# Kernel tuning notes

Hardware: AMD Instinct MI355X
Metric: run time of the kernel (lower is better)

## Reference

```python
import jax, jax.numpy as jnp
import numpy as np
from jax import lax

# 32 binary morphology kernels, row-major bit strings (kernel01..kernel800)
K3S = ["111001111", "111101101", "111100111", "101101111",
       "011101111", "111101011", "111101110", "110101111"]
K4S = ["0011000110011111", "1100100010011111", "1111100100010011", "1111100110001100",
       "1001100110011111", "1111000100011111", "1111100110011001", "1111100010001111"]
K5S = ["0001100001000011000111111", "1100010000100001000111111",
       "1111110001100001000011000", "1111110001000010000100011",
       "1111110000100001000011111", "1111100001000010000111111",
       "1111110001100011000110001", "1000110001100011000111111"]
K6S = ["000011000001000001000001100001111111", "110000100000100000100000100001111111",
       "111111100001100000100000100000110000", "111111100001000001000001000001000011",
       "111111100000100000100000100000111111", "111111000001000001000001000001111111",
       "111111100001100001100001100001100001", "100001100001100001100001100001111111"]

def _mk(strs, k):
    a = np.array([[int(c) for c in s] for s in strs], dtype=np.float32)
    return jnp.asarray(a.reshape(len(strs), 1, k, k))

# 'thick' mode: enumerate(start=1) vs set(range(32)) drops the LAST kernel (index 31)
GROUPS = [_mk(K3S, 3), _mk(K4S, 4), _mk(K5S, 5), _mk(K6S, 6)[:7]]

DIA = jnp.ones((1, 1, 3, 3), jnp.float32)
ERO = jnp.asarray([[0, 1, 0], [1, 0, 1], [0, 1, 0]], jnp.float32).reshape(1, 1, 3, 3)

def _conv(x, k, pad):
    return lax.conv_general_dilated(x, k, (1, 1), ((pad, pad), (pad, pad)),
                                    dimension_numbers=("NCHW", "OIHW", "NCHW"))

def _sig2(x, beta=0.5, alpha=10.0):
    # 1 / (1 + exp(-alpha*(x - beta)))
    return jax.nn.sigmoid(alpha * (x - beta))

def _endpoints_group(padded, kers):
    # batch all same-size kernels as output channels of one conv
    k = kers.shape[-1]
    pad = k // 2
    nc = _conv(padded, kers, pad)
    nc = nc[:, :, :padded.shape[2], :padded.shape[3]]  # crop (even-size kernels overshoot)
    # soft_threshold(nc, 1.0) * mask
    le = jax.nn.sigmoid(jnp.clip(-10.0 * (nc - 1.0), -10.0, 10.0)) * padded
    return le[:, :, 1:-1, 1:-1].sum(axis=1, keepdims=True)

def _cp_map(t):
    p = jnp.pad(t, ((0, 0), (0, 0), (1, 1), (1, 1)), constant_values=1.0)
    epss = _endpoints_group(p, GROUPS[0])
    for K in GROUPS[1:]:
        epss = epss + _endpoints_group(p, K)
    return _sig2(epss)

def _dilate(x):
    return jnp.clip(_conv(x, DIA, 1), 0.0, 1.0)

def _erode(x):
    t = _conv(x, ERO, 1)
    return _sig2(t / (t.max() + 1e-8), beta=0.7, alpha=10.0)

def _get_cp(t):
    return _dilate(_cp_map(t))

def _topo_loss(pred, gt, num_erosions):
    ge, pe = [gt], [pred]
    for _ in range(num_erosions):
        ge.append(_erode(ge[-1]))
        pe.append(_erode(pe[-1]))
    loss = jnp.float32(0.0)
    for i in range(num_erosions + 1):
        loss = loss + ((_get_cp(pe[i]) - _get_cp(ge[i])) ** 2).sum()
        loss = loss + ((_get_cp(pe[i].max() - pe[i]) - _get_cp(ge[i].max() - ge[i])) ** 2).sum()
    return loss / pred.shape[0]


def setup_inputs() -> dict:
    key = jax.random.key(0)
    k1, k2 = jax.random.split(key)
    B, H, W = 8, 512, 512
    pred = jax.random.uniform(k1, (B, 1, H, W), dtype=jnp.float32)
    gt = jax.random.uniform(k2, (B, 1, H, W), dtype=jnp.float32)
    return {"pred": pred, "gt": gt, "num_erosions": 2}


def reference(pred, gt, num_erosions):
    return _topo_loss(pred, gt, num_erosions)
```

## Files before the change

kernel.cpp:

```cpp
#include <hip/hip_runtime.h>
#include <hip/hip_fp16.h>
#include <cstdint>

static constexpr int B = 8;
static constexpr int H = 512;
static constexpr int W = 512;
static constexpr int HW = H * W;
static constexpr int NPIX = B * HW;
static constexpr int NB1 = 1024;
static constexpr int NBD = 1024;

static constexpr int N_INT = 30 * 14;
static constexpr int N_EDGE = 64 + 120;
static constexpr int GRID_X = N_INT + N_EDGE;

static constexpr float CC = 14.4269504088896f;

__device__ __forceinline__ float rcpf(float x) { return __builtin_amdgcn_rcpf(x); }
__device__ __forceinline__ float exp2f_n(float x) { return __builtin_amdgcn_exp2f(x); }

typedef __attribute__((ext_vector_type(2))) float f2;

__device__ __forceinline__ f2 mk2(float a, float b) { f2 r; r.x = a; r.y = b; return r; }
__device__ __forceinline__ f2 exp2_2(f2 v) {
    f2 r; r.x = exp2f_n(v.x); r.y = exp2f_n(v.y); return r;
}
__device__ __forceinline__ f2 rcp_2(f2 v) {
    f2 r; r.x = rcpf(v.x); r.y = rcpf(v.y); return r;
}
#if defined(__has_builtin)
#if __has_builtin(__builtin_elementwise_fma)
#define FMA2(a, b, c) __builtin_elementwise_fma((a), (b), (c))
#endif
#endif
#ifndef FMA2
__device__ __forceinline__ f2 fma2_(f2 a, f2 b, f2 c) {
    f2 r; r.x = fmaf(a.x, b.x, c.x); r.y = fmaf(a.y, b.y, c.y); return r;
}
#define FMA2(a, b, c) fma2_((a), (b), (c))
#endif

__device__ __forceinline__ float sig_cp(float x) {
    return rcpf(1.0f + exp2f_n(fmaf(x, -CC, 0.5f * CC)));
}
__device__ __forceinline__ float sig_er(float r) {
    return rcpf(1.0f + exp2f_n(fmaf(r, -CC, 0.7f * CC)));
}
__device__ __forceinline__ void pair_term2(f2 nc, f2 negA, f2 s2m,
                                           f2& sd, f2& sc) {
    const f2 CC2 = CC;
    const f2 one2 = 1.0f;
    f2 w = exp2_2(FMA2(nc, CC2, negA));
    sd += rcp_2(FMA2(w, s2m, one2));
    sc += w * rcp_2(w + s2m);
}
__device__ __forceinline__ void end_term2(f2 nc, f2& sd) {
    const f2 CC2 = CC;
    const f2 nCC2 = -CC;
    const f2 one2 = 1.0f;
    sd += rcp_2(one2 + exp2_2(FMA2(nc, CC2, nCC2)));
}
__device__ __forceinline__ float wave_max(float m) {
#pragma unroll
    for (int o = 32; o > 0; o >>= 1) m = fmaxf(m, __shfl_down(m, o, 64));
    return m;
}
__device__ __forceinline__ float wave_sum(float s) {
#pragma unroll
    for (int o = 32; o > 0; o >>= 1) s += __shfl_down(s, o, 64);
    return s;
}

union H4 {
    uint64_t u;
    __half2 h2[2];
    __half h[4];
};

__device__ __forceinline__ float4 h4_to_f4(uint64_t u) {
    H4 v; v.u = u;
    float2 p0 = __half22float2(v.h2[0]);
    float2 p1 = __half22float2(v.h2[1]);
    return make_float4(p0.x, p0.y, p1.x, p1.y);
}
__device__ __forceinline__ float4 f4_add(float4 a, float4 b) {
    return make_float4(a.x + b.x, a.y + b.y, a.z + b.z, a.w + b.w);
}

struct NC2 {
    f2 n3[8], n4[8], n5[8], n6[7];
    f2 v;
};

template <int STRIDE>
__device__ __forceinline__ NC2 sweep2(const f2* rp) {
    NC2 o;
    f2 r2s, r3s, r4s;
    f2 cen0, cen1, cen2, cen3, cen4, cen5, cen6, cen7, cen8;
    {
        f2 c0 = rp[0], c1 = rp[1], c2 = rp[2], c3 = rp[3], c4 = rp[4], c5 = rp[5];
        f2 c45 = c4 + c5, c01 = c0 + c1;
        f2 S6 = (c01 + (c2 + c3)) + c45;
        o.n6[0] = c45; o.n6[1] = c01; o.n6[2] = S6; o.n6[3] = S6;
        o.n6[4] = S6;  o.n6[5] = S6;  o.n6[6] = S6;
    }
    rp += STRIDE;
    {
        f2 c0 = rp[0], c1 = rp[1], c2 = rp[2], c3 = rp[3], c4 = rp[4], c5 = rp[5];
        f2 c45 = c4 + c5, c12 = c1 + c2, c34 = c3 + c4;
        f2 S4 = c12 + c34, S5 = S4 + c5;
        f2 c15 = c1 + c5, c05 = c0 + c5, c14 = c1 + c4;
        o.n6[0] += c5;  o.n6[1] += c0;  o.n6[2] += c05; o.n6[3] += c05;
        o.n6[4] += c0;  o.n6[5] += c5;  o.n6[6] += c05;
        o.n5[0] = c45; o.n5[1] = c12; o.n5[2] = S5; o.n5[3] = S5;
        o.n5[4] = S5;  o.n5[5] = S5;  o.n5[6] = S5; o.n5[7] = c15;
        o.n4[0] = c34; o.n4[1] = c12; o.n4[2] = S4; o.n4[3] = S4;
        o.n4[4] = c14; o.n4[5] = S4;  o.n4[6] = S4; o.n4[7] = S4;
    }
    rp += STRIDE;
    {
        f2 c0 = rp[0], c1 = rp[1], c2 = rp[2], c3 = rp[3], c4 = rp[4], c5 = rp[5];
        f2 c05 = c0 + c5, c15 = c1 + c5, c14 = c1 + c4;
        r2s = (c2 + c3) + c4;
        cen0 = c2; cen1 = c3; cen2 = c4;
        o.n6[0] += c5;  o.n6[1] += c0;  o.n6[2] += c0;  o.n6[3] += c5;
        o.n6[4] += c0;  o.n6[5] += c5;  o.n6[6] += c05;
        o.n5[0] += c5;  o.n5[1] += c1;  o.n5[2] += c15; o.n5[3] += c15;
        o.n5[4] += c1;  o.n5[5] += c5;  o.n5[6] += c15; o.n5[7] += c15;
        o.n4[0] += c4;  o.n4[1] += c1;  o.n4[2] += c14; o.n4[3] += c14;
        o.n4[4] += c14; o.n4[5] += c4;  o.n4[6] += c14; o.n4[7] += c1;
    }
    rp += STRIDE;
    {
        f2 c0 = rp[0], c1 = rp[1], c2 = rp[2], c3 = rp[3], c4 = rp[4], c5 = rp[5];
        f2 c05 = c0 + c5, c15 = c1 + c5, c14 = c1 + c4;
        r3s = (c2 + c3) + c4;
        cen3 = c2; cen4 = c3; cen5 = c4;
        o.v = c3;
        o.n6[0] += c5;  o.n6[1] += c0;  o.n6[2] += c0;  o.n6[3] += c5;
        o.n6[4] += c0;  o.n6[5] += c5;  o.n6[6] += c05;
        o.n5[0] += c5;  o.n5[1] += c1;  o.n5[2] += c1;  o.n5[3] += c5;
        o.n5[4] += c1;  o.n5[5] += c5;  o.n5[6] += c15; o.n5[7] += c15;
        o.n4[0] += c14; o.n4[1] += c14; o.n4[2] += c4;  o.n4[3] += c1;
        o.n4[4] += c14; o.n4[5] += c4;  o.n4[6] += c14; o.n4[7] += c1;
    }
    rp += STRIDE;
    {
        f2 c0 = rp[0], c1 = rp[1], c2 = rp[2], c3 = rp[3], c4 = rp[4], c5 = rp[5];
        f2 c05 = c0 + c5, c15 = c1 + c5, c12 = c1 + c2, c34 = c3 + c4;
        f2 S4 = c12 + c34, c14 = c1 + c4;
        r4s = (c2 + c3) + c4;
        cen6 = c2; cen7 = c3; cen8 = c4;
        o.n6[0] += c05; o.n6[1] += c05; o.n6[2] += c0;  o.n6[3] += c5;
        o.n6[4] += c0;  o.n6[5] += c5;  o.n6[6] += c05;
        o.n5[0] += c15; o.n5[1] += c15; o.n5[2] += c1;  o.n5[3] += c5;
        o.n5[4] += c1;  o.n5[5] += c5;  o.n5[6] += c15; o.n5[7] += c15;
        o.n4[0] += S4;  o.n4[1] += S4;  o.n4[2] += c34; o.n4[3] += c12;
        o.n4[4] += S4;  o.n4[5] += S4;  o.n4[6] += c14; o.n4[7] += S4;
    }
    rp += STRIDE;
    {
        f2 c0 = rp[0], c1 = rp[1], c2 = rp[2], c3 = rp[3], c4 = rp[4], c5 = rp[5];
        f2 c45 = c4 + c5, c12 = c1 + c2;
        f2 t = c3 + c45, S5 = c12 + t, S6 = S5 + c0;
        f2 c01 = c0 + c1, c05 = c0 + c5, c15 = c1 + c5;
        o.n6[0] += S6;  o.n6[1] += S6;  o.n6[2] += c01; o.n6[3] += c45;
        o.n6[4] += S6;  o.n6[5] += S6;  o.n6[6] += c05;
        o.n5[0] += S5;  o.n5[1] += S5;  o.n5[2] += c12; o.n5[3] += c45;
        o.n5[4] += S5;  o.n5[5] += S5;  o.n5[6] += c15; o.n5[7] += S5;
    }
    f2 S33 = (r2s + r3s) + r4s;
    f2 T = S33 - cen4;
    o.n3[0] = T - cen3; o.n3[1] = T - cen7; o.n3[2] = T - cen5; o.n3[3] = T - cen1;
    o.n3[4] = T - cen0; o.n3[5] = T - cen6; o.n3[6] = T - cen8; o.n3[7] = T - cen2;
    return o;
}

__constant__ __device__ const int CI4[8] = {1, 1, 1, 1, 2, 2, 2, 2};
__constant__ __device__ const int CI5[8] = {3, 3, 3, 3, 4, 4, 4, 4};
__constant__ __device__ const int CI6[7] = {4, 4, 4, 4, 5, 5, 5};

template <bool PAIR>
__device__ __forceinline__ void ssum_from_nc2(const NC2& a, const f2* negA,
                                              const f2* s2m, f2& sD, f2& sC) {
    f2 sd = 0.0f, sc = 0.0f;
#pragma unroll
    for (int k = 0; k < 8; k++) {
        if constexpr (PAIR) pair_term2(a.n3[k], negA[0], s2m[0], sd, sc);
        else end_term2(a.n3[k], sd);
    }
#pragma unroll
    for (int k = 0; k < 8; k++) {
        if constexpr (PAIR) pair_term2(a.n4[k], negA[CI4[k]], s2m[CI4[k]], sd, sc);
        else end_term2(a.n4[k], sd);
    }
#pragma unroll
    for (int k = 0; k < 8; k++) {
        if constexpr (PAIR) pair_term2(a.n5[k], negA[CI5[k]], s2m[CI5[k]], sd, sc);
        else end_term2(a.n5[k], sd);
    }
#pragma unroll
    for (int k = 0; k < 7; k++) {
        if constexpr (PAIR) pair_term2(a.n6[k], negA[CI6[k]], s2m[CI6[k]], sd, sc);
        else end_term2(a.n6[k], sd);
    }
    sD = sd;
    sC = sc;
}

__global__ __launch_bounds__(256, 4) void cp_main_kernel(
    const float* __restrict__ x0P, const float* __restrict__ x0G,
    const float* __restrict__ x1P, const float* __restrict__ x1G,
    const float* __restrict__ x2P, const float* __restrict__ x2G,
    const float* __restrict__ S, const float* __restrict__ CST,
    int lvl_base, int plane_lvl0, __half* __restrict__ cp) {
    __shared__ f2 win[37][23];
    const int lvl = lvl_base + (blockIdx.z >> 3);
    const int b = blockIdx.z & 7;
    const float* xP = (lvl == 0) ? x0P : (lvl == 1) ? x1P : x2P;
    const float* xG = (lvl == 0) ? x0G : (lvl == 1) ? x1G : x2G;
    const float MP = S[lvl], MG = S[3 + lvl];
    __half* cpb = cp + (size_t)(4 * (lvl - plane_lvl0)) * NPIX;
    const int tid = threadIdx.y * 16 + threadIdx.x;
    const int ty = threadIdx.y, tx = threadIdx.x;
    const f2* cbase = (const f2*)(CST + lvl * 24);

    if (blockIdx.x < N_INT) {
        const int txB = 1 + (int)blockIdx.x % 30;
        const int tyB = 1 + (int)blockIdx.x / 30;
        const int ox0 = txB * 16, oy0 = tyB * 32;
        const float* pb = xP + b * HW + (oy0 - 3) * W + (ox0 - 3);
        const float* gb = xG + b * HW + (oy0 - 3) * W + (ox0 - 3);
        {
            int i = tid, r = tid / 21, c = tid - (tid / 21) * 21;
            while (i < 37 * 21) {
                win[r][c] = mk2(pb[r * W + c], gb[r * W + c]);
                i += 256; c += 4; r += 12;
                if (c >= 21) { c -= 21; r += 1; }
            }
        }
        __syncthreads();
        f2 negA[6], s2m[6];
#pragma unroll
        for (int c = 0; c < 6; c++) { negA[c] = cbase[c]; s2m[c] = cbase[6 + c]; }
        int o = b * HW + (oy0 + ty) * W + (ox0 + tx);
        {
            f2 sd, sc;
            NC2 a = sweep2<23>(&win[ty][tx]);
            ssum_from_nc2<true>(a, negA, s2m, sd, sc);
            H4 v;
            v.h[0] = __float2half(sig_cp(a.v.x * sd.x));
            v.h[1] = __float2half(sig_cp(a.v.y * sd.y));
            v.h[2] = __float2half(sig_cp((MP - a.v.x) * sc.x));
            v.h[3] = __float2half(sig_cp((MG - a.v.y) * sc.y));
            *(uint64_t*)(cpb + (size_t)o * 4) = v.u;
        }
        o += 16 * W;
        {
            f2 sd, sc;
            NC2 a = sweep2<23>(&win[ty + 16][tx]);
            ssum_from_nc2<true>(a, negA, s2m, sd, sc);
            H4 v;
            v.h[0] = __float2half(sig_cp(a.v.x * sd.x));
            v.h[1] = __float2half(sig_cp(a.v.y * sd.y));
            v.h[2] = __float2half(sig_cp((MP - a.v.x) * sc.x));
            v.h[3] = __float2half(sig_cp((MG - a.v.y) * sc.y));
            *(uint64_t*)(cpb + (size_t)o * 4) = v.u;
        }
    } else {
        const int e = (int)blockIdx.x - N_INT;
        int tx16, ty16;
        if (e < 64) {
            ty16 = e >> 1;
            tx16 = (e & 1) ? 31 : 0;
        } else {
            int e2 = e - 64;
            int r = e2 / 30;
            ty16 = (r == 0) ? 0 : (r == 1) ? 1 : (r == 2) ? 30 : 31;
            tx16 = 1 + e2 % 30;
        }
        const int ox0 = tx16 * 16, oy0 = ty16 * 16;
        const int o = b * HW + (oy0 + ty) * W + (ox0 + tx);
        const bool fastw = (tx16 >= 1) & (tx16 <= 30) & (ty16 >= 1) & (ty16 <= 30);
        if (fastw) {
            const float* pb = xP + b * HW + (oy0 - 3) * W + (ox0 - 3);
            const float* gb = xG + b * HW + (oy0 - 3) * W + (ox0 - 3);
            {
                int i = tid, r = tid / 21, c = tid - (tid / 21) * 21;
                while (i < 21 * 21) {
                    win[r][c] = mk2(pb[r * W + c], gb[r * W + c]);
                    i += 256; c += 4; r += 12;
                    if (c >= 21) { c -= 21; r += 1; }
                }
            }
            __syncthreads();
            f2 negA[6], s2m[6], sd, sc;
#pragma unroll
            for (int c = 0; c < 6; c++) { negA[c] = cbase[c]; s2m[c] = cbase[6 + c]; }
            NC2 a = sweep2<23>(&win[ty][tx]);
            ssum_from_nc2<true>(a, negA, s2m, sd, sc);
            H4 v;
            v.h[0] = __float2half(sig_cp(a.v.x * sd.x));
            v.h[1] = __float2half(sig_cp(a.v.y * sd.y));
            v.h[2] = __float2half(sig_cp((MP - a.v.x) * sc.x));
            v.h[3] = __float2half(sig_cp((MG - a.v.y) * sc.y));
            *(uint64_t*)(cpb + (size_t)o * 4) = v.u;
        } else {
            const float* pb = xP + b * HW;
            const float* gb = xG + b * HW;
            {
                int i = tid, r = tid / 21, c = tid - (tid / 21) * 21;
                while (i < 21 * 21) {
                    int pr = oy0 - 2 + r;
                    int pc = ox0 - 2 + c;
                    f2 v;
                    if (pr < 0 || pr > H + 1 || pc < 0 || pc > W + 1) {
                        v = 0.0f;
                    } else if (pr == 0 || pr == H + 1 || pc == 0 || pc == W + 1) {
                        v = 1.0f;
                    } else {
                        v = mk2(pb[(pr - 1) * W + (pc - 1)], gb[(pr - 1) * W + (pc - 1)]);
                    }
                    win[r][c] = v;
                    i += 256; c += 4; r += 12;
                    if (c >= 21) { c -= 21; r += 1; }
                }
            }
            __syncthreads();
            f2 sd, sc, junk;
            NC2 a = sweep2<23>(&win[ty][tx]);
            ssum_from_nc2<false>(a, nullptr, nullptr, sd, junk);
            f2 vD = a.v;
            __half2* po = (__half2*)(cpb + (size_t)o * 4);
            po[0] = __halves2half2(__float2half(sig_cp(vD.x * sd.x)),
                                   __float2half(sig_cp(vD.y * sd.y)));
            __syncthreads();
            {
                int i = tid, r = tid / 21, c = tid - (tid / 21) * 21;
                while (i < 21 * 21) {
                    int pr = oy0 - 2 + r;
                    int pc = ox0 - 2 + c;
                    f2 v;
                    if (pr < 0 || pr > H + 1 || pc < 0 || pc > W + 1) {
                        v = 0.0f;
                    } else if (pr == 0 || pr == H + 1 || pc == 0 || pc == W + 1) {
                        v = 1.0f;
                    } else {
                        v = mk2(MP - pb[(pr - 1) * W + (pc - 1)],
                                MG - gb[(pr - 1) * W + (pc - 1)]);
                    }
                    win[r][c] = v;
                    i += 256; c += 4; r += 12;
                    if (c >= 21) { c -= 21; r += 1; }
                }
            }
            __syncthreads();
            NC2 ac = sweep2<23>(&win[ty][tx]);
            ssum_from_nc2<false>(ac, nullptr, nullptr, sc, junk);
            po[1] = __halves2half2(__float2half(sig_cp(ac.v.x * sc.x)),
                                   __float2half(sig_cp(ac.v.y * sc.y)));
        }
    }
}

__global__ __launch_bounds__(256, 4) void dil_diff2_kernel(
    const __half* __restrict__ cp, float* __restrict__ partial) {
    const int plane_grp = blockIdx.x >> 9;
    const int r = blockIdx.x & 511;
    const __half* cpb = cp + (size_t)(4 * plane_grp) * NPIX;
    const int x0 = threadIdx.x << 1;
    const int y0 = (r & 63) << 3;
    const int b = r >> 6;
    const __half* pb = cpb + (size_t)b * HW * 4;

    float4 ring0[3], ring1[3];
    float s = 0.0f;
#pragma unroll
    for (int j = 0; j < 10; j++) {
        int yy = y0 - 1 + j;
        float4 a0 = make_float4(0.f, 0.f, 0.f, 0.f);
        float4 a1 = a0;
        if (yy >= 0 && yy < H) {
            const __half* row = pb + (size_t)yy * (W * 4);
            float4 f0 = h4_to_f4(*(const uint64_t*)(row + (size_t)x0 * 4));
            float4 f1 = h4_to_f4(*(const uint64_t*)(row + (size_t)(x0 + 1) * 4));
            float4 lf = make_float4(0.f, 0.f, 0.f, 0.f), rt = lf;
            if (x0 > 0)
                lf = h4_to_f4(*(const uint64_t*)(row + (size_t)(x0 - 1) * 4));
            if (x0 + 2 < W)
                rt = h4_to_f4(*(const uint64_t*)(row + (size_t)(x0 + 2) * 4));
            a0 = f4_add(f4_add(lf, f0), f1);
            a1 = f4_add(f4_add(f0, f1), rt);
        }
        ring0[j % 3] = a0; ring1[j % 3] = a1;
        if (j >= 2) {
            float4 v0 = f4_add(f4_add(ring0[(j - 2) % 3], ring0[(j - 1) % 3]),
                               ring0[j % 3]);
            float4 v1 = f4_add(f4_add(ring1[(j - 2) % 3], ring1[(j - 1) % 3]),
                               ring1[j % 3]);
            float d1 = fminf(v0.x, 1.0f) - fminf(v0.y, 1.0f);
            float d2 = fminf(v0.z, 1.0f) - fminf(v0.w, 1.0f);
            s += fmaf(d1, d1, d2 * d2);
            d1 = fminf(v1.x, 1.0f) - fminf(v1.y, 1.0f);
            d2 = fminf(v1.z, 1.0f) - fminf(v1.w, 1.0f);
            s += fmaf(d1, d1, d2 * d2);
        }
    }
    s = wave_sum(s);
    __shared__ float red[4];
    int tid = threadIdx.x;
    if ((tid & 63) == 0) red[tid >> 6] = s;
    __syncthreads();
    if (tid == 0) partial[blockIdx.x] = (red[0] + red[1]) + (red[2] + red[3]);
}

__device__ __forceinline__ void cross4(const float* __restrict__ xp, int idx,
                                       int y, int c, float4& ctr, float t[4]) {
    const float4* v = (const float4*)(xp + idx);
    ctr = v[0];
    float4 up = (y > 0) ? *(const float4*)(xp + idx - W)
                        : make_float4(0, 0, 0, 0);
    float4 dn = (y < H - 1) ? *(const float4*)(xp + idx + W)
                            : make_float4(0, 0, 0, 0);
    float lf = (c > 0) ? xp[idx - 1] : 0.0f;
    float rt = (c < W - 4) ? xp[idx + 4] : 0.0f;
    t[0] = (up.x + dn.x) + (lf + ctr.y);
    t[1] = (up.y + dn.y) + (ctr.x + ctr.z);
    t[2] = (up.z + dn.z) + (ctr.y + ctr.w);
    t[3] = (up.w + dn.w) + (ctr.z + rt);
}

__device__ __forceinline__ void cross_lds(const float* rm1, const float* r0,
                                          const float* rp1, int col,
                                          float4& ctr, float t[4]) {
    ctr = *(const float4*)(r0 + col);
    float4 up = *(const float4*)(rm1 + col);
    float4 dn = *(const float4*)(rp1 + col);
    float lf = (col > 0) ? r0[col - 1] : 0.0f;
    float rt = (col < W - 4) ? r0[col + 4] : 0.0f;
    t[0] = (up.x + dn.x) + (lf + ctr.y);
    t[1] = (up.y + dn.y) + (ctr.x + ctr.z);
    t[2] = (up.z + dn.z) + (ctr.y + ctr.w);
    t[3] = (up.w + dn.w) + (ctr.z + rt);
}

__global__ __launch_bounds__(256) void cross_max_both_kernel(
    const float* __restrict__ xP, const float* __restrict__ xG,
    float4* __restrict__ partial) {
    float mtP = 0, mtG = 0, mrP = 0, mrG = 0;
    for (int T = blockIdx.x * 256 + threadIdx.x; T < NPIX / 4; T += NB1 * 256) {
        int idx = T * 4;
        int i = idx & (HW - 1);
        int y = i >> 9;
        int c = i & (W - 1);
        float4 ctr;
        float t[4];
        cross4(xP, idx, y, c, ctr, t);
        mtP = fmaxf(mtP, fmaxf(fmaxf(t[0], t[1]), fmaxf(t[2], t[3])));
        mrP = fmaxf(mrP, fmaxf(fmaxf(ctr.x, ctr.y), fmaxf(ctr.z, ctr.w)));
        cross4(xG, idx, y, c, ctr, t);
        mtG = fmaxf(mtG, fmaxf(fmaxf(t[0], t[1]), fmaxf(t[2], t[3])));
        mrG = fmaxf(mrG, fmaxf(fmaxf(ctr.x, ctr.y), fmaxf(ctr.z, ctr.w)));
    }
    mtP = wave_max(mtP); mtG = wave_max(mtG);
    mrP = wave_max(mrP); mrG = wave_max(mrG);
    __shared__ float red[4][4];
    int tid = threadIdx.x;
    if ((tid & 63) == 0) {
        int w = tid >> 6;
        red[w][0] = mtP; red[w][1] = mtG; red[w][2] = mrP; red[w][3] = mrG;
    }
    __syncthreads();
    if (tid == 0) {
        float4 r;
        r.x = fmaxf(fmaxf(red[0][0], red[1][0]), fmaxf(red[2][0], red[3][0]));
        r.y = fmaxf(fmaxf(red[0][1], red[1][1]), fmaxf(red[2][1], red[3][1]));
        r.z = fmaxf(fmaxf(red[0][2], red[1][2]), fmaxf(red[2][2], red[3][2]));
        r.w = fmaxf(fmaxf(red[0][3], red[1][3]), fmaxf(red[2][3], red[3][3]));
        partial[blockIdx.x] = r;
    }
}

__global__ __launch_bounds__(256) void erode_cmax_kernel(
    const float* __restrict__ xP, const float* __restrict__ xG,
    const float4* __restrict__ PM1,
    float* __restrict__ yP, float* __restrict__ yG,
    float4* __restrict__ PMo, float* __restrict__ S) {
    __shared__ float lyP[6][W], lyG[6][W];
    __shared__ float red[4][4];
    const int tid = threadIdx.x;
    const int b = blockIdx.x >> 7;
    const int y0 = ((int)blockIdx.x & 127) << 2;

    float a = 0, bm = 0, c4 = 0, d4 = 0;
#pragma unroll
    for (int k = 0; k < NB1 / 256; k++) {
        float4 p = PM1[tid + k * 256];
        a = fmaxf(a, p.x); bm = fmaxf(bm, p.y);
        c4 = fmaxf(c4, p.z); d4 = fmaxf(d4, p.w);
    }
    a = wave_max(a); bm = wave_max(bm); c4 = wave_max(c4); d4 = wave_max(d4);
    if ((tid & 63) == 0) {
        int w = tid >> 6;
        red[w][0] = a; red[w][1] = bm; red[w][2] = c4; red[w][3] = d4;
    }
    __syncthreads();
    a  = fmaxf(fmaxf(red[0][0], red[1][0]), fmaxf(red[2][0], red[3][0]));
    bm = fmaxf(fmaxf(red[0][1], red[1][1]), fmaxf(red[2][1], red[3][1]));
    c4 = fmaxf(fmaxf(red[0][2], red[1][2]), fmaxf(red[2][2], red[3][2]));
    d4 = fmaxf(fmaxf(red[0][3], red[1][3]), fmaxf(red[2][3], red[3][3]));
    const float invP = rcpf(a + 1e-8f);
    const float invG = rcpf(bm + 1e-8f);

    for (int t = tid; t < 6 * 128; t += 256) {
        int ri = t >> 7;
        int col = (t & 127) << 2;
        int yy = y0 - 1 + ri;
        float4 oP = make_float4(0.f, 0.f, 0.f, 0.f), oG = oP;
        if (yy >= 0 && yy < H) {
            int idx = b * HW + yy * W + col;
            float4 ctr; float tv[4];
            cross4(xP, idx, yy, col, ctr, tv);
            oP = make_float4(sig_er(tv[0] * invP), sig_er(tv[1] * invP),
                             sig_er(tv[2] * invP), sig_er(tv[3] * invP));
            cross4(xG, idx, yy, col, ctr, tv);
            oG = make_float4(sig_er(tv[0] * invG), sig_er(tv[1] * invG),
                             sig_er(tv[2] * invG), sig_er(tv[3] * invG));
            if (ri >= 1 && ri <= 4) {
                *(float4*)(yP + idx) = oP;
                *(float4*)(yG + idx) = oG;
            }
        }
        *(float4*)(&lyP[ri][col]) = oP;
        *(float4*)(&lyG[ri][col]) = oG;
    }
    __syncthreads();

    float mtP = 0, mtG = 0, mrP = 0, mrG = 0;
    for (int t = tid; t < 4 * 128; t += 256) {
        int rj = 1 + (t >> 7);
        int col = (t & 127) << 2;
        float4 ctr; float tv[4];
        cross_lds(lyP[rj - 1], lyP[rj], lyP[rj + 1], col, ctr, tv);
        mtP = fmaxf(mtP, fmaxf(fmaxf(tv[0], tv[1]), fmaxf(tv[2], tv[3])));
        mrP = fmaxf(mrP, fmaxf(fmaxf(ctr.x, ctr.y), fmaxf(ctr.z, ctr.w)));
        cross_lds(lyG[rj - 1], lyG[rj], lyG[rj + 1], col, ctr, tv);
        mtG = fmaxf(mtG, fmaxf(fmaxf(tv[0], tv[1]), fmaxf(tv[2], tv[3])));
        mrG = fmaxf(mrG, fmaxf(fmaxf(ctr.x, ctr.y), fmaxf(ctr.z, ctr.w)));
    }
    mtP = wave_max(mtP); mtG = wave_max(mtG);
    mrP = wave_max(mrP); mrG = wave_max(mrG);
    __syncthreads();
    if ((tid & 63) == 0) {
        int w = tid >> 6;
        red[w][0] = mtP; red[w][1] = mtG; red[w][2] = mrP; red[w][3] = mrG;
    }
    __syncthreads();
    if (tid == 0) {
        float4 r;
        r.x = fmaxf(fmaxf(red[0][0], red[1][0]), fmaxf(red[2][0], red[3][0]));
        r.y = fmaxf(fmaxf(red[0][1], red[1][1]), fmaxf(red[2][1], red[3][1]));
        r.z = fmaxf(fmaxf(red[0][2], red[1][2]), fmaxf(red[2][2], red[3][2]));
        r.w = fmaxf(fmaxf(red[0][3], red[1][3]), fmaxf(red[2][3], red[3][3]));
        PMo[blockIdx.x] = r;
        if (blockIdx.x == 0) {
            S[1] = sig_er(a * invP);
            S[4] = sig_er(bm * invG);
            S[0] = c4;
            S[3] = d4;
        }
    }
}

__global__ __launch_bounds__(256) void erode_both_kernel(
    const float* __restrict__ xP, const float* __restrict__ xG,
    const float4* __restrict__ PM,
    float* __restrict__ yP, float* __restrict__ yG,
    float* ymaxP, float* ymaxG, float* rmaxP, float* rmaxG,
    const float* __restrict__ Sg, float* __restrict__ CST) {
    float a = 0, bm = 0, c4 = 0, d4 = 0;
    {
        int t = threadIdx.x;
#pragma unroll
        for (int k = 0; k < NB1 / 256; k++) {
            float4 p = PM[t + k * 256];
            a = fmaxf(a, p.x); bm = fmaxf(bm, p.y);
            c4 = fmaxf(c4, p.z); d4 = fmaxf(d4, p.w);
        }
        a = wave_max(a); bm = wave_max(bm); c4 = wave_max(c4); d4 = wave_max(d4);
        __shared__ float red[4][4];
        if ((t & 63) == 0) {
            int w = t >> 6;
            red[w][0] = a; red[w][1] = bm; red[w][2] = c4; red[w][3] = d4;
        }
        __syncthreads();
        a  = fmaxf(fmaxf(red[0][0], red[1][0]), fmaxf(red[2][0], red[3][0]));
        bm = fmaxf(fmaxf(red[0][1], red[1][1]), fmaxf(red[2][1], red[3][1]));
        c4 = fmaxf(fmaxf(red[0][2], red[1][2]), fmaxf(red[2][2], red[3][2]));
        d4 = fmaxf(fmaxf(red[0][3], red[1][3]), fmaxf(red[2][3], red[3][3]));
    }
    const float tP_max = a, tG_max = bm;
    const float invP = rcpf(tP_max + 1e-8f);
    const float invG = rcpf(tG_max + 1e-8f);

    const int T = blockIdx.x * 256 + threadIdx.x;
    if (T < NPIX / 4) {
        int idx = T * 4;
        int i = idx & (HW - 1);
        int y = i >> 9;
        int c = i & (W - 1);
        float4 ctr;
        float t[4], o[4];
        cross4(xP, idx, y, c, ctr, t);
#pragma unroll
        for (int k = 0; k < 4; k++) o[k] = sig_er(t[k] * invP);
        *(float4*)(yP + idx) = make_float4(o[0], o[1], o[2], o[3]);
        cross4(xG, idx, y, c, ctr, t);
#pragma unroll
        for (int k = 0; k < 4; k++) o[k] = sig_er(t[k] * invG);
        *(float4*)(yG + idx) = make_float4(o[0], o[1], o[2], o[3]);
    }
    if (blockIdx.x == 0) {
        if (threadIdx.x == 0) {
            *ymaxP = sig_er(tP_max * invP);
            *ymaxG = sig_er(tG_max * invG);
            *rmaxP = c4;
            *rmaxG = d4;
        }
        if (threadIdx.x < 36) {
            int t = threadIdx.x;
            int lvl = t / 12, rem = t % 12, cls = rem >> 1, img = rem & 1;
            const float cntf[6] = {7.0f, 9.0f, 10.0f, 11.0f, 13.0f, 16.0f};
            float M;
            if (lvl == 2)
                M = img ? sig_er(tG_max * invG) : sig_er(tP_max * invP);
            else
                M = Sg[lvl + 3 * img];
            float cm = fmaf(cntf[cls] * M, CC, -CC);
            float m = 0.5f * (cm - CC);
            CST[lvl * 24 + cls * 2 + img] = -(CC + m);
            CST[lvl * 24 + 12 + cls * 2 + img] = exp2f_n(m);
        }
    }
}

__global__ __launch_bounds__(1024) void finalize_kernel(
    const float* __restrict__ PS, float* out) {
    int t = threadIdx.x;
    float s = PS[t] + ((t < 512) ? PS[t + 1024] : 0.0f);
    s = wave_sum(s);
    __shared__ float red[16];
    if ((t & 63) == 0) red[t >> 6] = s;
    __syncthreads();
    if (t == 0) {
        float tot = 0.0f;
#pragma unroll
        for (int i = 0; i < 16; i++) tot += red[i];
        out[0] = tot * (1.0f / (float)B);
    }
}

extern "C" void kernel_launch(void* const* d_in, const int* in_sizes, int n_in,
                              void* d_out, int out_size, void* d_ws, size_t ws_size,
                              hipStream_t stream) {
    (void)in_sizes; (void)n_in; (void)out_size;
    const float* pred = (const float*)d_in[0];
    const float* gt   = (const float*)d_in[1];
    float* out = (float*)d_out;

    float* S  = (float*)d_ws;
    float4* PM = (float4*)(S + 64);
    float* PS = S + 64 + 4 * NB1;
    float* CST = PS + 2560;
    float* P1 = PS + 3 * NBD;
    float* G1 = P1 + NPIX;
    float* P2 = G1 + NPIX;
    float* G2 = P2 + NPIX;
    __half* CP = (__half*)(G2 + NPIX);
    float4* PM2 = (float4*)CP;

    const size_t base_b = (size_t)(64 + 4 * NB1 + 3 * NBD) * 4 +
                          (size_t)4 * NPIX * 4;
    const bool merged = ws_size >= base_b + (size_t)12 * NPIX * 2;

    const dim3 b1(256), g1(NB1), gE(NPIX / 4 / 256);
    const dim3 b2(16, 16, 1);

    cross_max_both_kernel<<<g1, b1, 0, stream>>>(pred, gt, PM);
    erode_cmax_kernel<<<dim3(NB1), b1, 0, stream>>>(pred, gt, PM, P1, G1,
                                                    PM2, S);
    erode_both_kernel<<<gE, b1, 0, stream>>>(P1, G1, PM2, P2, G2,
                                             S + 2, S + 5, S + 12, S + 13,
                                             S, CST);

    if (merged) {
        cp_main_kernel<<<dim3(GRID_X, 1, 3 * B), b2, 0, stream>>>(
            pred, gt, P1, G1, P2, G2, S, CST, 0, 0, CP);
        dil_diff2_kernel<<<dim3(3 * 512), b1, 0, stream>>>(CP, PS);
    } else {
        for (int lvl = 0; lvl < 3; lvl++) {
            cp_main_kernel<<<dim3(GRID_X, 1, B), b2, 0, stream>>>(
                pred, gt, P1, G1, P2, G2, S, CST, lvl, lvl, CP);
            dil_diff2_kernel<<<dim3(512), b1, 0, stream>>>(CP, PS + lvl * 512);
        }
    }

    finalize_kernel<<<1, 1024, 0, stream>>>(PS, out);
}
```

Baseline: 251.6 us.

## Fuse second erosion into cp_main tile loads, dropping erode_both kernel

Removes the separate kernel that materialised the second-level eroded images P2/G2. For level 2, cp_main now reduces the per-block maxima itself and computes the erosion on the fly while filling its shared-memory window. The per-level pair constants are also derived in-block. This saves a full-image write and read pass plus one launch, at the cost of redundant erosion arithmetic and extra halo gathers in every level-2 block, plus a small per-block max reduction.

```diff
diff --git a/kernel.cpp b/kernel.cpp
--- a/kernel.cpp
+++ b/kernel.cpp
@@ -85,6 +85,20 @@
 }
 __device__ __forceinline__ float4 f4_add(float4 a, float4 b) {
     return make_float4(a.x + b.x, a.y + b.y, a.z + b.z, a.w + b.w);
+}
+
+__device__ __forceinline__ float erode_at(const float* __restrict__ p,
+                                          int y, int x, float inv) {
+    int i = y * W + x;
+    float up = (y > 0) ? p[i - W] : 0.0f;
+    float dn = (y < H - 1) ? p[i + W] : 0.0f;
+    float lf = (x > 0) ? p[i - 1] : 0.0f;
+    float rt = (x < W - 1) ? p[i + 1] : 0.0f;
+    return sig_er(((up + dn) + (lf + rt)) * inv);
+}
+__device__ __forceinline__ float erode_at_i(const float* __restrict__ p,
+                                            int i, float inv) {
+    return sig_er(((p[i - W] + p[i + W]) + (p[i - 1] + p[i + 1])) * inv);
 }
 
 struct NC2 {
@@ -208,22 +222,64 @@
     sC = sc;
 }
 
+__device__ __forceinline__ void pair_const(float cnt, float M,
+                                           float& negA, float& s2m) {
+    float cm = fmaf(cnt * M, CC, -CC);
+    float m = 0.5f * (cm - CC);
+    negA = -(CC + m);
+    s2m = exp2f_n(m);
+}
+
 __global__ __launch_bounds__(256, 4) void cp_main_kernel(
     const float* __restrict__ x0P, const float* __restrict__ x0G,
     const float* __restrict__ x1P, const float* __restrict__ x1G,
-    const float* __restrict__ x2P, const float* __restrict__ x2G,
+    const float4* __restrict__ PM2,
     const float* __restrict__ S, const float* __restrict__ CST,
     int lvl_base, int plane_lvl0, __half* __restrict__ cp) {
     __shared__ f2 win[37][23];
+    __shared__ float redc[4][2];
     const int lvl = lvl_base + (blockIdx.z >> 3);
     const int b = blockIdx.z & 7;
-    const float* xP = (lvl == 0) ? x0P : (lvl == 1) ? x1P : x2P;
-    const float* xG = (lvl == 0) ? x0G : (lvl == 1) ? x1G : x2G;
-    const float MP = S[lvl], MG = S[3 + lvl];
+    const bool l2 = (lvl == 2);
+    const float* xP = (lvl == 0) ? x0P : x1P;
+    const float* xG = (lvl == 0) ? x0G : x1G;
     __half* cpb = cp + (size_t)(4 * (lvl - plane_lvl0)) * NPIX;
     const int tid = threadIdx.y * 16 + threadIdx.x;
     const int ty = threadIdx.y, tx = threadIdx.x;
-    const f2* cbase = (const f2*)(CST + lvl * 24);
+
+    float MP, MG, invP2 = 0.0f, invG2 = 0.0f;
+    f2 negA[6], s2m[6];
+    if (!l2) {
+        MP = S[lvl]; MG = S[3 + lvl];
+        const f2* cbase = (const f2*)(CST + lvl * 24);
+#pragma unroll
+        for (int c = 0; c < 6; c++) { negA[c] = cbase[c]; s2m[c] = cbase[6 + c]; }
+    } else {
+        float a = 0.0f, bm = 0.0f;
+#pragma unroll
+        for (int k = 0; k < NB1 / 256; k++) {
+            float4 p = PM2[tid + k * 256];
+            a = fmaxf(a, p.x); bm = fmaxf(bm, p.y);
+        }
+        a = wave_max(a); bm = wave_max(bm);
+        if ((tid & 63) == 0) { redc[tid >> 6][0] = a; redc[tid >> 6][1] = bm; }
+        __syncthreads();
+        a  = fmaxf(fmaxf(redc[0][0], redc[1][0]), fmaxf(redc[2][0], redc[3][0]));
+        bm = fmaxf(fmaxf(redc[0][1], redc[1][1]), fmaxf(redc[2][1], redc[3][1]));
+        invP2 = rcpf(a + 1e-8f);
+        invG2 = rcpf(bm + 1e-8f);
+        MP = sig_er(a * invP2);
+        MG = sig_er(bm * invG2);
+        const float cntf[6] = {7.0f, 9.0f, 10.0f, 11.0f, 13.0f, 16.0f};
+#pragma unroll
+        for (int c = 0; c < 6; c++) {
+            float nP, sP, nG, sG;
+            pair_const(cntf[c], MP, nP, sP);
+            pair_const(cntf[c], MG, nG, sG);
+            negA[c] = mk2(nP, nG);
+            s2m[c] = mk2(sP, sG);
+        }
+    }
 
     if (blockIdx.x < N_INT) {
         const int txB = 1 + (int)blockIdx.x % 30;
@@ -231,18 +287,24 @@
         const int ox0 = txB * 16, oy0 = tyB * 32;
         const float* pb = xP + b * HW + (oy0 - 3) * W + (ox0 - 3);
         const float* gb = xG + b * HW + (oy0 - 3) * W + (ox0 - 3);
-        {
+        if (!l2) {
             int i = tid, r = tid / 21, c = tid - (tid / 21) * 21;
             while (i < 37 * 21) {
                 win[r][c] = mk2(pb[r * W + c], gb[r * W + c]);
                 i += 256; c += 4; r += 12;
                 if (c >= 21) { c -= 21; r += 1; }
             }
+        } else {
+            int i = tid, r = tid / 21, c = tid - (tid / 21) * 21;
+            while (i < 37 * 21) {
+                int idx = r * W + c;
+                win[r][c] = mk2(erode_at_i(pb, idx, invP2),
+                                erode_at_i(gb, idx, invG2));
+                i += 256; c += 4; r += 12;
+                if (c >= 21) { c -= 21; r += 1; }
+            }
         }
         __syncthreads();
-        f2 negA[6], s2m[6];
-#pragma unroll
-        for (int c = 0; c < 6; c++) { negA[c] = cbase[c]; s2m[c] = cbase[6 + c]; }
         int o = b * HW + (oy0 + ty) * W + (ox0 + tx);
         {
             f2 sd, sc;
@@ -285,18 +347,25 @@
         if (fastw) {
             const float* pb = xP + b * HW + (oy0 - 3) * W + (ox0 - 3);
             const float* gb = xG + b * HW + (oy0 - 3) * W + (ox0 - 3);
-            {
+            if (!l2) {
                 int i = tid, r = tid / 21, c = tid - (tid / 21) * 21;
                 while (i < 21 * 21) {
                     win[r][c] = mk2(pb[r * W + c], gb[r * W + c]);
                     i += 256; c += 4; r += 12;
                     if (c >= 21) { c -= 21; r += 1; }
                 }
+            } else {
+                int i = tid, r = tid / 21, c = tid - (tid / 21) * 21;
+                while (i < 21 * 21) {
+                    int idx = r * W + c;
+                    win[r][c] = mk2(erode_at_i(pb, idx, invP2),
+                                    erode_at_i(gb, idx, invG2));
+                    i += 256; c += 4; r += 12;
+                    if (c >= 21) { c -= 21; r += 1; }
+                }
             }
             __syncthreads();
-            f2 negA[6], s2m[6], sd, sc;
-#pragma unroll
-            for (int c = 0; c < 6; c++) { negA[c] = cbase[c]; s2m[c] = cbase[6 + c]; }
+            f2 sd, sc;
             NC2 a = sweep2<23>(&win[ty][tx]);
             ssum_from_nc2<true>(a, negA, s2m, sd, sc);
             H4 v;
@@ -318,8 +387,11 @@
                         v = 0.0f;
                     } else if (pr == 0 || pr == H + 1 || pc == 0 || pc == W + 1) {
                         v = 1.0f;
+                    } else if (!l2) {
+                        v = mk2(pb[(pr - 1) * W + (pc - 1)], gb[(pr - 1) * W + (pc - 1)]);
                     } else {
-                        v = mk2(pb[(pr - 1) * W + (pc - 1)], gb[(pr - 1) * W + (pc - 1)]);
+                        v = mk2(erode_at(pb, pr - 1, pc - 1, invP2),
+                                erode_at(gb, pr - 1, pc - 1, invG2));
                     }
                     win[r][c] = v;
                     i += 256; c += 4; r += 12;
@@ -345,9 +417,12 @@
                         v = 0.0f;
                     } else if (pr == 0 || pr == H + 1 || pc == 0 || pc == W + 1) {
                         v = 1.0f;
-                    } else {
+                    } else if (!l2) {
                         v = mk2(MP - pb[(pr - 1) * W + (pc - 1)],
                                 MG - gb[(pr - 1) * W + (pc - 1)]);
+                    } else {
+                        v = mk2(MP - erode_at(pb, pr - 1, pc - 1, invP2),
+                                MG - erode_at(gb, pr - 1, pc - 1, invG2));
                     }
                     win[r][c] = v;
                     i += 256; c += 4; r += 12;
@@ -485,7 +560,8 @@
     const float* __restrict__ xP, const float* __restrict__ xG,
     const float4* __restrict__ PM1,
     float* __restrict__ yP, float* __restrict__ yG,
-    float4* __restrict__ PMo, float* __restrict__ S) {
+    float4* __restrict__ PMo, float* __restrict__ S,
+    float* __restrict__ CST) {
     __shared__ float lyP[6][W], lyG[6][W];
     __shared__ float red[4][4];
     const int tid = threadIdx.x;
@@ -563,83 +639,23 @@
         r.z = fmaxf(fmaxf(red[0][2], red[1][2]), fmaxf(red[2][2], red[3][2]));
         r.w = fmaxf(fmaxf(red[0][3], red[1][3]), fmaxf(red[2][3], red[3][3]));
         PMo[blockIdx.x] = r;
-        if (blockIdx.x == 0) {
+    }
+    if (blockIdx.x == 0) {
+        if (tid == 0) {
             S[1] = sig_er(a * invP);
             S[4] = sig_er(bm * invG);
             S[0] = c4;
             S[3] = d4;
         }
-    }
-}
-
-__global__ __launch_bounds__(256) void erode_both_kernel(
-    const float* __restrict__ xP, const float* __restrict__ xG,
-    const float4* __restrict__ PM,
-    float* __restrict__ yP, float* __restrict__ yG,
-    float* ymaxP, float* ymaxG, float* rmaxP, float* rmaxG,
-    const float* __restrict__ Sg, float* __restrict__ CST) {
-    float a = 0, bm = 0, c4 = 0, d4 = 0;
-    {
-        int t = threadIdx.x;
-#pragma unroll
-        for (int k = 0; k < NB1 / 256; k++) {
-            float4 p = PM[t + k * 256];
-            a = fmaxf(a, p.x); bm = fmaxf(bm, p.y);
-            c4 = fmaxf(c4, p.z); d4 = fmaxf(d4, p.w);
-        }
-        a = wave_max(a); bm = wave_max(bm); c4 = wave_max(c4); d4 = wave_max(d4);
-        __shared__ float red[4][4];
-        if ((t & 63) == 0) {
-            int w = t >> 6;
-            red[w][0] = a; red[w][1] = bm; red[w][2] = c4; red[w][3] = d4;
-        }
-        __syncthreads();
-        a  = fmaxf(fmaxf(red[0][0], red[1][0]), fmaxf(red[2][0], red[3][0]));
-        bm = fmaxf(fmaxf(red[0][1], red[1][1]), fmaxf(red[2][1], red[3][1]));
-        c4 = fmaxf(fmaxf(red[0][2], red[1][2]), fmaxf(red[2][2], red[3][2]));
-        d4 = fmaxf(fmaxf(red[0][3], red[1][3]), fmaxf(red[2][3], red[3][3]));
-    }
-    const float tP_max = a, tG_max = bm;
-    const float invP = rcpf(tP_max + 1e-8f);
-    const float invG = rcpf(tG_max + 1e-8f);
-
-    const int T = blockIdx.x * 256 + threadIdx.x;
-    if (T < NPIX / 4) {
-        int idx = T * 4;
-        int i = idx & (HW - 1);
-        int y = i >> 9;
-        int c = i & (W - 1);
-        float4 ctr;
-        float t[4], o[4];
-        cross4(xP, idx, y, c, ctr, t);
-#pragma unroll
-        for (int k = 0; k < 4; k++) o[k] = sig_er(t[k] * invP);
-        *(float4*)(yP + idx) = make_float4(o[0], o[1], o[2], o[3]);
-        cross4(xG, idx, y, c, ctr, t);
-#pragma unroll
-        for (int k = 0; k < 4; k++) o[k] = sig_er(t[k] * invG);
-        *(float4*)(yG + idx) = make_float4(o[0], o[1], o[2], o[3]);
-    }
-    if (blockIdx.x == 0) {
-        if (threadIdx.x == 0) {
-            *ymaxP = sig_er(tP_max * invP);
-            *ymaxG = sig_er(tG_max * invG);
-            *rmaxP = c4;
-            *rmaxG = d4;
-        }
-        if (threadIdx.x < 36) {
-            int t = threadIdx.x;
-            int lvl = t / 12, rem = t % 12, cls = rem >> 1, img = rem & 1;
+        if (tid < 24) {
+            int lvl = tid / 12, rem = tid % 12, cls = rem >> 1, img = rem & 1;
             const float cntf[6] = {7.0f, 9.0f, 10.0f, 11.0f, 13.0f, 16.0f};
-            float M;
-            if (lvl == 2)
-                M = img ? sig_er(tG_max * invG) : sig_er(tP_max * invP);
-            else
-                M = Sg[lvl + 3 * img];
-            float cm = fmaf(cntf[cls] * M, CC, -CC);
-            float m = 0.5f * (cm - CC);
-            CST[lvl * 24 + cls * 2 + img] = -(CC + m);
-            CST[lvl * 24 + 12 + cls * 2 + img] = exp2f_n(m);
+            float M = (lvl == 0) ? (img ? d4 : c4)
+                                 : (img ? sig_er(bm * invG) : sig_er(a * invP));
+            float nA, sM;
+            pair_const(cntf[cls], M, nA, sM);
+            CST[lvl * 24 + cls * 2 + img] = nA;
+            CST[lvl * 24 + 12 + cls * 2 + img] = sM;
         }
     }
 }
@@ -674,33 +690,30 @@
     float* CST = PS + 2560;
     float* P1 = PS + 3 * NBD;
     float* G1 = P1 + NPIX;
-    float* P2 = G1 + NPIX;
-    float* G2 = P2 + NPIX;
-    __half* CP = (__half*)(G2 + NPIX);
-    float4* PM2 = (float4*)CP;
+    float* P2slot = G1 + NPIX;
+    float* G2slot = P2slot + NPIX;
+    __half* CP = (__half*)(G2slot + NPIX);
+    float4* PM2 = (float4*)P2slot;
 
     const size_t base_b = (size_t)(64 + 4 * NB1 + 3 * NBD) * 4 +
                           (size_t)4 * NPIX * 4;
     const bool merged = ws_size >= base_b + (size_t)12 * NPIX * 2;
 
-    const dim3 b1(256), g1(NB1), gE(NPIX / 4 / 256);
+    const dim3 b1(256), g1(NB1);
     const dim3 b2(16, 16, 1);
 
     cross_max_both_kernel<<<g1, b1, 0, stream>>>(pred, gt, PM);
     erode_cmax_kernel<<<dim3(NB1), b1, 0, stream>>>(pred, gt, PM, P1, G1,
-                                                    PM2, S);
-    erode_both_kernel<<<gE, b1, 0, stream>>>(P1, G1, PM2, P2, G2,
-                                             S + 2, S + 5, S + 12, S + 13,
-                                             S, CST);
+                                                    PM2, S, CST);
 
     if (merged) {
         cp_main_kernel<<<dim3(GRID_X, 1, 3 * B), b2, 0, stream>>>(
-            pred, gt, P1, G1, P2, G2, S, CST, 0, 0, CP);
+            pred, gt, P1, G1, PM2, S, CST, 0, 0, CP);
         dil_diff2_kernel<<<dim3(3 * 512), b1, 0, stream>>>(CP, PS);
     } else {
         for (int lvl = 0; lvl < 3; lvl++) {
             cp_main_kernel<<<dim3(GRID_X, 1, B), b2, 0, stream>>>(
-                pred, gt, P1, G1, P2, G2, S, CST, lvl, lvl, CP);
+                pred, gt, P1, G1, PM2, S, CST, lvl, lvl, CP);
             dil_diff2_kernel<<<dim3(512), b1, 0, stream>>>(CP, PS + lvl * 512);
         }
     }
```

After: 263.8 us. +4.9%, slower.
